# Optimization experiments

Measured on AMD Instinct MI355X. Metric: run time of the kernel, lower is better.

Reference implementation:

```python
import jax, jax.numpy as jnp
import numpy as np

N_ATOMS = 100000
N_EDGES = 6400000
R_MAX = 6.0
KE = 14.3996


def inverse_softplus(x):
    return np.log(np.expm1(x))


def setup_inputs() -> dict:
    key = jax.random.key(0)
    k_r, k_z, k_i, k_j = jax.random.split(key, 4)
    R = jax.random.normal(k_r, (N_ATOMS, 3), dtype=jnp.float32) * 10.0
    Z = jax.random.randint(k_z, (N_ATOMS,), 1, 50, dtype=jnp.int32)
    idx_i = jax.random.randint(k_i, (N_EDGES,), 0, N_ATOMS, dtype=jnp.int32)
    idx_j = jax.random.randint(k_j, (N_EDGES,), 0, N_ATOMS, dtype=jnp.int32)
    idx = jnp.stack([idx_i, idx_j], axis=0)  # [2, E]
    box = jnp.zeros((3,), dtype=jnp.float32)
    offsets = jnp.zeros((N_EDGES, 3), dtype=jnp.float32)
    # learned params stored in inverse-softplus space, as in setup()
    a_exp = jnp.full((1,), inverse_softplus(0.23), dtype=jnp.float32)
    a_num = jnp.full((1,), inverse_softplus(0.4685), dtype=jnp.float32)
    coefficients = jnp.asarray(
        inverse_softplus(np.array([0.18175, 0.50986, 0.28022, 0.02817])[:, None]),
        dtype=jnp.float32)
    exponents = jnp.asarray(
        inverse_softplus(np.array([3.1998, 0.94229, 0.4029, 0.20162])[:, None]),
        dtype=jnp.float32)
    rep_scale = jnp.full((1,), inverse_softplus(1.0 / KE), dtype=jnp.float32)
    return {"R": R, "Z": Z, "idx": idx, "box": box, "offsets": offsets,
            "a_exp": a_exp, "a_num": a_num, "coefficients": coefficients,
            "exponents": exponents, "rep_scale": rep_scale}


def reference(R, Z, idx, box, offsets, a_exp, a_num, coefficients, exponents, rep_scale):
    idx_i, idx_j = idx[0], idx[1]
    Zf = Z.astype(R.dtype)
    Z_i = Zf[idx_i]  # [E]
    Z_j = Zf[idx_j]  # [E]
    # free-space displacement: R[idx_j] - R[idx_i]  (box/offsets unused)
    dr_vec = R[idx_j] - R[idx_i]                     # [E, 3]
    dr = jnp.sqrt(jnp.sum(dr_vec * dr_vec, axis=-1))  # [E]
    dr = jnp.clip(dr, 0.02, R_MAX)
    cos_cutoff = 0.5 * (jnp.cos(np.pi * dr / R_MAX) + 1.0)
    sp = jax.nn.softplus
    ae = sp(a_exp)           # (1,)
    an = sp(a_num)           # (1,)
    c = sp(coefficients)     # (4, 1)
    e = sp(exponents)        # (4, 1)
    rs = sp(rep_scale)       # (1,)
    a_divisor = Z_i ** ae + Z_j ** ae              # [E]
    dist = dr * a_divisor / an                     # [E]
    f = jnp.sum(c * jnp.exp(-e * dist), axis=0)    # (4,E) -> [E]
    E_ij = Z_i * Z_j / dr * f * cos_cutoff         # [E]
    mask = (idx_i != idx_j).astype(E_ij.dtype)     # padded self-edges masked
    E = 0.5 * rs * KE * jnp.sum(E_ij * mask)       # (1,)
    return jnp.sum(E)                              # scalar
```

## Files before the change

kernel.cpp:

```cpp
#include <hip/hip_runtime.h>

#ifndef KE_CONST
#define KE_CONST 14.3996f
#endif

constexpr float LOG2E = 1.4426950408889634f;
constexpr float LN2 = 0.6931471805599453f;

typedef int vint4 __attribute__((ext_vector_type(4)));

__device__ __forceinline__ float fast_exp2(float x) { return __builtin_amdgcn_exp2f(x); }
__device__ __forceinline__ float fast_log2(float x) { return __builtin_amdgcn_logf(x); }
__device__ __forceinline__ float fast_exp(float x) { return __builtin_amdgcn_exp2f(x * LOG2E); }
__device__ __forceinline__ float cos_rev(float rev) { return __builtin_amdgcn_cosf(rev); }
__device__ __forceinline__ float fast_sqrt(float x) { return __builtin_amdgcn_sqrtf(x); }
__device__ __forceinline__ float fast_rcp(float x) { return __builtin_amdgcn_rcpf(x); }

__device__ __forceinline__ float softplus_f(float x) {
    return LN2 * fast_log2(1.0f + fast_exp(x));
}

__device__ __forceinline__ float to_sgpr(float x) {
    return __uint_as_float((unsigned)__builtin_amdgcn_readfirstlane((int)__float_as_uint(x)));
}

__global__ void pack_atoms_kernel(const float* __restrict__ R,
                                  const int* __restrict__ Z,
                                  float4* __restrict__ atoms, int n,
                                  float* __restrict__ out) {
    int t = blockIdx.x * blockDim.x + threadIdx.x;
    if (t == 0) out[0] = 0.0f;
    if (t < n) {
        atoms[t] = make_float4(R[3 * t + 0], R[3 * t + 1], R[3 * t + 2],
                               (float)Z[t]);
    }
}

__global__ __launch_bounds__(256, 4) void edge_energy_kernel(
    const int* __restrict__ idx,
    const float4* __restrict__ atoms,
    const float* __restrict__ a_exp, const float* __restrict__ a_num,
    const float* __restrict__ coefficients, const float* __restrict__ exponents,
    const float* __restrict__ rep_scale,
    float* __restrict__ out, int nEdges) {
    __shared__ float zpow_lut[64];
    __shared__ float smem[4];

    const long long tid = (long long)blockIdx.x * blockDim.x + threadIdx.x;
    const long long base = tid * 8;
    const bool full = (base + 8 <= (long long)nEdges);

    vint4 ia, ib, ja, jb;
    if (full) {
        const vint4* __restrict__ i4 = (const vint4*)(idx) + (base >> 2);
        const vint4* __restrict__ j4 = (const vint4*)(idx + nEdges) + (base >> 2);
        ia = i4[0];
        ib = i4[1];
        ja = j4[0];
        jb = j4[1];
    }

    {
        const float ae = softplus_f(a_exp[0]);
        if (threadIdx.x < 64) {
            float z = (float)(threadIdx.x == 0 ? 1 : threadIdx.x);
            zpow_lut[threadIdx.x] = fast_exp2(ae * fast_log2(z));
        }
    }
    __syncthreads();

    float4 A[8], B[8];
    unsigned live = 0;
    float acc = 0.0f;

    if (full) {
        int ii[8] = {ia.x, ia.y, ia.z, ia.w, ib.x, ib.y, ib.z, ib.w};
        int jj[8] = {ja.x, ja.y, ja.z, ja.w, jb.x, jb.y, jb.z, jb.w};
#pragma unroll
        for (int u = 0; u < 8; ++u) live |= (ii[u] != jj[u] ? 1u : 0u) << u;
#pragma unroll
        for (int u = 0; u < 8; ++u) {
            A[u] = atoms[ii[u]];
            B[u] = atoms[jj[u]];
        }
        __builtin_amdgcn_sched_barrier(0);
    }

    const float inv_an = to_sgpr(fast_rcp(softplus_f(a_num[0])));
    const float c0 = to_sgpr(softplus_f(coefficients[0]));
    const float c1 = to_sgpr(softplus_f(coefficients[1]));
    const float c2 = to_sgpr(softplus_f(coefficients[2]));
    const float c3 = to_sgpr(softplus_f(coefficients[3]));
    const float e0 = to_sgpr(softplus_f(exponents[0]));
    const float e1 = to_sgpr(softplus_f(exponents[1]));
    const float e2 = to_sgpr(softplus_f(exponents[2]));
    const float e3 = to_sgpr(softplus_f(exponents[3]));
    const float scale = to_sgpr(0.5f * softplus_f(rep_scale[0]) * KE_CONST);

    if (full) {
#pragma unroll
        for (int u = 0; u < 8; ++u) {
            float dx = B[u].x - A[u].x;
            float dy = B[u].y - A[u].y;
            float dz = B[u].z - A[u].z;
            float dr2 = dx * dx + dy * dy + dz * dz;
            if (dr2 < 36.0f && ((live >> u) & 1u)) {
                float dr = fmaxf(fast_sqrt(dr2), 0.02f);
                float cc = 0.5f * (cos_rev(dr * (1.0f / 12.0f)) + 1.0f);
                float zpi = zpow_lut[(int)A[u].w];
                float zpj = zpow_lut[(int)B[u].w];
                float dist = dr * (zpi + zpj) * inv_an;
                float f = c0 * fast_exp(-e0 * dist) + c1 * fast_exp(-e1 * dist) +
                          c2 * fast_exp(-e2 * dist) + c3 * fast_exp(-e3 * dist);
                acc += A[u].w * B[u].w * fast_rcp(dr) * f * cc;
            }
        }
    } else if (base < (long long)nEdges) {
        for (long long t = base; t < (long long)nEdges; ++t) {
            int i = idx[t], j = idx[nEdges + t];
            float4 ai = atoms[i];
            float4 aj = atoms[j];
            float dx = aj.x - ai.x;
            float dy = aj.y - ai.y;
            float dz = aj.z - ai.z;
            float dr2 = dx * dx + dy * dy + dz * dz;
            if (dr2 < 36.0f && i != j) {
                float dr = fmaxf(fast_sqrt(dr2), 0.02f);
                float cc = 0.5f * (cos_rev(dr * (1.0f / 12.0f)) + 1.0f);
                float zpi = zpow_lut[(int)ai.w];
                float zpj = zpow_lut[(int)aj.w];
                float dist = dr * (zpi + zpj) * inv_an;
                float f = c0 * fast_exp(-e0 * dist) + c1 * fast_exp(-e1 * dist) +
                          c2 * fast_exp(-e2 * dist) + c3 * fast_exp(-e3 * dist);
                acc += ai.w * aj.w * fast_rcp(dr) * f * cc;
            }
        }
    }

#pragma unroll
    for (int off = 32; off > 0; off >>= 1) acc += __shfl_down(acc, off, 64);
    const int lane = threadIdx.x & 63;
    const int wave = threadIdx.x >> 6;
    if (lane == 0) smem[wave] = acc;
    __syncthreads();
    if (threadIdx.x == 0) {
        float s = (smem[0] + smem[1]) + (smem[2] + smem[3]);
        atomicAdd(out, s * scale);
    }
}

extern "C" void kernel_launch(void* const* d_in, const int* in_sizes, int n_in,
                              void* d_out, int out_size, void* d_ws, size_t ws_size,
                              hipStream_t stream) {
    const float* R = (const float*)d_in[0];
    const int* Z = (const int*)d_in[1];
    const int* idx = (const int*)d_in[2];
    const float* a_exp = (const float*)d_in[5];
    const float* a_num = (const float*)d_in[6];
    const float* coefficients = (const float*)d_in[7];
    const float* exponents = (const float*)d_in[8];
    const float* rep_scale = (const float*)d_in[9];

    const int nAtoms = in_sizes[0] / 3;
    const int nEdges = in_sizes[2] / 2;
    float* out = (float*)d_out;

    float4* atoms = (float4*)d_ws;
    pack_atoms_kernel<<<(nAtoms + 255) / 256, 256, 0, stream>>>(R, Z, atoms,
                                                                nAtoms, out);
    const int edges_per_block = 256 * 8;
    const int blocks = (nEdges + edges_per_block - 1) / edges_per_block;
    edge_energy_kernel<<<blocks, 256, 0, stream>>>(
        idx, atoms, a_exp, a_num, coefficients, exponents, rep_scale, out,
        nEdges);
}
```

Measured before the change: 198.5 us.

## Use persistent grid-stride edge loop with index prefetch and inline Z-power

The edge kernel becomes a persistent grid-stride loop over 1024 blocks instead of one 8-edge chunk per thread. While the current chunk's atom gathers are in flight, it prefetches the index vectors for the next chunk. The shared-memory Z^a lookup table and its __syncthreads are replaced by per-edge log2/exp2 evaluation, and the per-block atomic count drops. The tail edges go to a single thread. The cost is extra transcendental work per edge, and fewer waves may in flight to hide gather latency.

New measurement: 198.0 us. No clear change (-0.2%).

```diff
diff --git a/kernel.cpp b/kernel.cpp
--- a/kernel.cpp
+++ b/kernel.cpp
@@ -43,49 +43,13 @@
     const float* __restrict__ coefficients, const float* __restrict__ exponents,
     const float* __restrict__ rep_scale,
     float* __restrict__ out, int nEdges) {
-    __shared__ float zpow_lut[64];
     __shared__ float smem[4];
 
-    const long long tid = (long long)blockIdx.x * blockDim.x + threadIdx.x;
-    const long long base = tid * 8;
-    const bool full = (base + 8 <= (long long)nEdges);
+    const int S = gridDim.x * blockDim.x;
+    const int tid = blockIdx.x * blockDim.x + threadIdx.x;
+    const int nChunks = nEdges >> 3;
 
-    vint4 ia, ib, ja, jb;
-    if (full) {
-        const vint4* __restrict__ i4 = (const vint4*)(idx) + (base >> 2);
-        const vint4* __restrict__ j4 = (const vint4*)(idx + nEdges) + (base >> 2);
-        ia = i4[0];
-        ib = i4[1];
-        ja = j4[0];
-        jb = j4[1];
-    }
-
-    {
-        const float ae = softplus_f(a_exp[0]);
-        if (threadIdx.x < 64) {
-            float z = (float)(threadIdx.x == 0 ? 1 : threadIdx.x);
-            zpow_lut[threadIdx.x] = fast_exp2(ae * fast_log2(z));
-        }
-    }
-    __syncthreads();
-
-    float4 A[8], B[8];
-    unsigned live = 0;
-    float acc = 0.0f;
-
-    if (full) {
-        int ii[8] = {ia.x, ia.y, ia.z, ia.w, ib.x, ib.y, ib.z, ib.w};
-        int jj[8] = {ja.x, ja.y, ja.z, ja.w, jb.x, jb.y, jb.z, jb.w};
-#pragma unroll
-        for (int u = 0; u < 8; ++u) live |= (ii[u] != jj[u] ? 1u : 0u) << u;
-#pragma unroll
-        for (int u = 0; u < 8; ++u) {
-            A[u] = atoms[ii[u]];
-            B[u] = atoms[jj[u]];
-        }
-        __builtin_amdgcn_sched_barrier(0);
-    }
-
+    const float ae     = to_sgpr(softplus_f(a_exp[0]));
     const float inv_an = to_sgpr(fast_rcp(softplus_f(a_num[0])));
     const float c0 = to_sgpr(softplus_f(coefficients[0]));
     const float c1 = to_sgpr(softplus_f(coefficients[1]));
@@ -97,7 +61,39 @@
     const float e3 = to_sgpr(softplus_f(exponents[3]));
     const float scale = to_sgpr(0.5f * softplus_f(rep_scale[0]) * KE_CONST);
 
-    if (full) {
+    float acc = 0.0f;
+
+    int c = tid;
+    vint4 ia, ib, ja, jb;
+    if (c < nChunks) {
+        const vint4* __restrict__ i4 = (const vint4*)(idx) + (c << 1);
+        const vint4* __restrict__ j4 = (const vint4*)(idx + nEdges) + (c << 1);
+        ia = i4[0]; ib = i4[1]; ja = j4[0]; jb = j4[1];
+    }
+
+    while (c < nChunks) {
+        int ii[8] = {ia.x, ia.y, ia.z, ia.w, ib.x, ib.y, ib.z, ib.w};
+        int jj[8] = {ja.x, ja.y, ja.z, ja.w, jb.x, jb.y, jb.z, jb.w};
+        unsigned live = 0;
+#pragma unroll
+        for (int u = 0; u < 8; ++u) live |= (ii[u] != jj[u] ? 1u : 0u) << u;
+
+        float4 A[8], B[8];
+#pragma unroll
+        for (int u = 0; u < 8; ++u) {
+            A[u] = atoms[ii[u]];
+            B[u] = atoms[jj[u]];
+        }
+        __builtin_amdgcn_sched_barrier(0);
+
+        const int cn = c + S;
+        if (cn < nChunks) {
+            const vint4* __restrict__ i4 = (const vint4*)(idx) + (cn << 1);
+            const vint4* __restrict__ j4 = (const vint4*)(idx + nEdges) + (cn << 1);
+            ia = i4[0]; ib = i4[1]; ja = j4[0]; jb = j4[1];
+        }
+        __builtin_amdgcn_sched_barrier(0);
+
 #pragma unroll
         for (int u = 0; u < 8; ++u) {
             float dx = B[u].x - A[u].x;
@@ -107,16 +103,19 @@
             if (dr2 < 36.0f && ((live >> u) & 1u)) {
                 float dr = fmaxf(fast_sqrt(dr2), 0.02f);
                 float cc = 0.5f * (cos_rev(dr * (1.0f / 12.0f)) + 1.0f);
-                float zpi = zpow_lut[(int)A[u].w];
-                float zpj = zpow_lut[(int)B[u].w];
+                float zpi = fast_exp2(ae * fast_log2(A[u].w));
+                float zpj = fast_exp2(ae * fast_log2(B[u].w));
                 float dist = dr * (zpi + zpj) * inv_an;
                 float f = c0 * fast_exp(-e0 * dist) + c1 * fast_exp(-e1 * dist) +
                           c2 * fast_exp(-e2 * dist) + c3 * fast_exp(-e3 * dist);
                 acc += A[u].w * B[u].w * fast_rcp(dr) * f * cc;
             }
         }
-    } else if (base < (long long)nEdges) {
-        for (long long t = base; t < (long long)nEdges; ++t) {
+        c = cn;
+    }
+
+    if (tid == 0) {
+        for (int t = nChunks << 3; t < nEdges; ++t) {
             int i = idx[t], j = idx[nEdges + t];
             float4 ai = atoms[i];
             float4 aj = atoms[j];
@@ -127,8 +126,8 @@
             if (dr2 < 36.0f && i != j) {
                 float dr = fmaxf(fast_sqrt(dr2), 0.02f);
                 float cc = 0.5f * (cos_rev(dr * (1.0f / 12.0f)) + 1.0f);
-                float zpi = zpow_lut[(int)ai.w];
-                float zpj = zpow_lut[(int)aj.w];
+                float zpi = fast_exp2(ae * fast_log2(ai.w));
+                float zpj = fast_exp2(ae * fast_log2(aj.w));
                 float dist = dr * (zpi + zpj) * inv_an;
                 float f = c0 * fast_exp(-e0 * dist) + c1 * fast_exp(-e1 * dist) +
                           c2 * fast_exp(-e2 * dist) + c3 * fast_exp(-e3 * dist);
@@ -168,8 +167,12 @@
     float4* atoms = (float4*)d_ws;
     pack_atoms_kernel<<<(nAtoms + 255) / 256, 256, 0, stream>>>(R, Z, atoms,
                                                                 nAtoms, out);
-    const int edges_per_block = 256 * 8;
-    const int blocks = (nEdges + edges_per_block - 1) / edges_per_block;
+
+    const int nChunks = nEdges >> 3;
+    int blocks = 1024;
+    const int maxNeeded = (nChunks + 255) / 256;
+    if (blocks > maxNeeded) blocks = maxNeeded;
+    if (blocks < 1) blocks = 1;
     edge_energy_kernel<<<blocks, 256, 0, stream>>>(
         idx, atoms, a_exp, a_num, coefficients, exponents, rep_scale, out,
         nEdges);
```
